# Kernel tuning notes

Hardware: AMD Instinct MI355X
Metric: run time of the kernel (lower is better)

Reference implementation:

```python
import jax, jax.numpy as jnp
import numpy as np

# NOTE: in the original SelfAttention.forward, the selected/softmaxed/dropped
# attention `attn` is NEVER used: the output is `torch.matmul(attn_cont, value)`
# with the RAW pre-mask, pre-softmax, unscaled scores. The AutoSelectAttention /
# softmax / dropout branch is dead code w.r.t. the module output, so the faithful
# forward is out = proj_out( (Q K^T) V ) per head.

B, M, HID, K = 2, 2048, 1024, 16
D = HID // K


def setup_inputs() -> dict:
    key = jax.random.key(0)
    ks = jax.random.split(key, 6)
    s = 1.0 / np.sqrt(HID)
    return {
        "h": jax.random.normal(ks[0], (B, M, HID), jnp.float32),
        "Wq": jax.random.normal(ks[1], (HID, HID), jnp.float32) * s,
        "Wk": jax.random.normal(ks[2], (HID, HID), jnp.float32) * s,
        "Wv": jax.random.normal(ks[3], (HID, HID), jnp.float32) * s,
        "Wspan": jax.random.normal(ks[4], (2 * K, HID), jnp.float32) * s,
        "Wo": jax.random.normal(ks[5], (HID, HID), jnp.float32) * s,
    }


def _heads(x, d):
    # [B, M, K*d] -> [B, K, M, d]
    b, m, _ = x.shape
    return x.reshape(b, m, K, d).transpose(0, 2, 1, 3)


def reference(h, Wq, Wk, Wv, Wspan, Wo):
    # torch Linear: y = x @ W.T  (weights stored [out, in])
    q = _heads(h @ Wq.T, D)          # [B,K,M,D]
    k = _heads(h @ Wk.T, D)          # [B,K,M,D]
    v = _heads(h @ Wv.T, D)          # [B,K,M,D]
    span = _heads(h @ Wspan.T, 2)    # [B,K,M,2] -- dead code in original, kept for parity
    del span
    # raw scores (attn_cont in the original)
    scores = jnp.einsum("bkmd,bknd->bkmn", q, k)      # [B,K,M,M]
    # original: out = attn_cont @ value (select/softmax branch unused)
    out = jnp.einsum("bkmn,bknd->bkmd", scores, v)    # [B,K,M,D]
    out = out.transpose(0, 2, 1, 3).reshape(B, M, HID)
    return out @ Wo.T
```

## Files before the change

### kernel.cpp

```cpp
#include <hip/hip_runtime.h>
#include <hip/hip_bf16.h>
#include <stdint.h>

typedef __hip_bfloat16 bf16_t;
typedef __attribute__((ext_vector_type(8))) __bf16 bf16x8;
typedef __attribute__((ext_vector_type(4))) float floatx4;

#define BM 128
#define BN 128
#define BK 64

__device__ inline void async_load16(const void* g, void* l) {
  __builtin_amdgcn_global_load_lds(
      (const __attribute__((address_space(1))) unsigned int*)g,
      (__attribute__((address_space(3))) unsigned int*)l,
      16, 0, 0);
}

__device__ inline void unpack8_bf16(float* dst, uint4 u) {
  const unsigned w[4] = {u.x, u.y, u.z, u.w};
#pragma unroll
  for (int p = 0; p < 4; ++p) {
    dst[2 * p]     = __uint_as_float(w[p] << 16);
    dst[2 * p + 1] = __uint_as_float(w[p] & 0xffff0000u);
  }
}

__device__ inline unsigned short bf16_bits(float f) {
  bf16_t b = __float2bfloat16(f);
  return *(const unsigned short*)&b;
}

__global__ void cvt_one(const float* __restrict__ src, bf16_t* __restrict__ dst) {
  const int i = (blockIdx.x * 256 + threadIdx.x) * 4;
  float4 f = *(const float4*)(src + i);
  union { unsigned short u[4]; uint2 v; } p;
  p.u[0] = bf16_bits(f.x); p.u[1] = bf16_bits(f.y);
  p.u[2] = bf16_bits(f.z); p.u[3] = bf16_bits(f.w);
  *(uint2*)(dst + i) = p.v;
}

__global__ void cvt_w4(const float* __restrict__ s0, const float* __restrict__ s1,
                       const float* __restrict__ s2, const float* __restrict__ s3,
                       bf16_t* __restrict__ d0, bf16_t* __restrict__ d1,
                       bf16_t* __restrict__ d2, bf16_t* __restrict__ d3) {
  const float* s; bf16_t* d;
  switch (blockIdx.y) {
    case 0: s = s0; d = d0; break;
    case 1: s = s1; d = d1; break;
    case 2: s = s2; d = d2; break;
    default: s = s3; d = d3; break;
  }
  const int i = (blockIdx.x * 256 + threadIdx.x) * 4;
  float4 f = *(const float4*)(s + i);
  union { unsigned short u[4]; uint2 v; } p;
  p.u[0] = bf16_bits(f.x); p.u[1] = bf16_bits(f.y);
  p.u[2] = bf16_bits(f.z); p.u[3] = bf16_bits(f.w);
  *(uint2*)(d + i) = p.v;
}

template <typename OutT>
__global__ __launch_bounds__(256, 2)
void gemm_nt(const bf16_t* __restrict__ A, int lda,
             const bf16_t* __restrict__ B0, const bf16_t* __restrict__ B1,
             const bf16_t* __restrict__ B2,
             OutT* __restrict__ C, int ldc, int Kdim)
{
  __shared__ alignas(16) __bf16 As[BM * BK];
  __shared__ alignas(16) __bf16 Bs[BN * BK];

  const int t = threadIdx.x;
  const int lane = t & 63;
  const int wave = t >> 6;
  const int wm = wave >> 1;
  const int wn = wave & 1;

  const int m0 = blockIdx.x * BM;
  const int nblk = blockIdx.y * BN;
  const int mat = nblk >> 10;
  const bf16_t* __restrict__ B = (mat == 0) ? B0 : ((mat == 1) ? B1 : B2);
  const int n0 = nblk & 1023;

  floatx4 acc[4][4];
#pragma unroll
  for (int i = 0; i < 4; ++i)
#pragma unroll
    for (int j = 0; j < 4; ++j)
      acc[i][j] = (floatx4){0.f, 0.f, 0.f, 0.f};

  const int srow = t >> 3;
  const int sgs = t & 7;

  for (int k0 = 0; k0 < Kdim; k0 += BK) {
#pragma unroll
    for (int r4 = 0; r4 < 4; ++r4) {
      const int row = r4 * 32 + srow;
      const int gsrc = sgs ^ (row & 7);
      async_load16(A + (size_t)(m0 + row) * lda + k0 + gsrc * 8,
                   &As[row * BK + sgs * 8]);
      async_load16(B + (size_t)(n0 + row) * Kdim + k0 + gsrc * 8,
                   &Bs[row * BK + sgs * 8]);
    }
    __syncthreads();
#pragma unroll
    for (int ks = 0; ks < 2; ++ks) {
      bf16x8 af[4], bfv[4];
#pragma unroll
      for (int i = 0; i < 4; ++i) {
        const int row = wm * 64 + i * 16 + (lane & 15);
        const int g = ks * 4 + (lane >> 4);
        af[i] = *(const bf16x8*)&As[row * BK + (g ^ (row & 7)) * 8];
      }
#pragma unroll
      for (int j = 0; j < 4; ++j) {
        const int row = wn * 64 + j * 16 + (lane & 15);
        const int g = ks * 4 + (lane >> 4);
        bfv[j] = *(const bf16x8*)&Bs[row * BK + (g ^ (row & 7)) * 8];
      }
#pragma unroll
      for (int i = 0; i < 4; ++i)
#pragma unroll
        for (int j = 0; j < 4; ++j)
          acc[i][j] = __builtin_amdgcn_mfma_f32_16x16x32_bf16(
              af[i], bfv[j], acc[i][j], 0, 0, 0);
    }
    __syncthreads();
  }

  const int ccol = lane & 15;
  const int crow = (lane >> 4) * 4;
#pragma unroll
  for (int i = 0; i < 4; ++i) {
#pragma unroll
    for (int j = 0; j < 4; ++j) {
      const int gcol = nblk + wn * 64 + j * 16 + ccol;
      const int growb = m0 + wm * 64 + i * 16 + crow;
#pragma unroll
      for (int r = 0; r < 4; ++r) {
        float v = acc[i][j][r];
        if constexpr (__is_same(OutT, bf16_t))
          C[(size_t)(growb + r) * ldc + gcol] = __float2bfloat16(v);
        else
          C[(size_t)(growb + r) * ldc + gcol] = v;
      }
    }
  }
}

__global__ __launch_bounds__(256)
void ktv_kernel(const bf16_t* __restrict__ qkv, float* __restrict__ S)
{
  __shared__ float Kf[32][64];
  __shared__ float Vf[32][64];
  const int bh = blockIdx.x;
  const int b = bh >> 4, hh = bh & 15;
  const int mc = blockIdx.y;
  const int t = threadIdx.x;
  const int d0 = (t & 15) * 4;
  const int e0 = (t >> 4) * 4;

  const bf16_t* kbase = qkv + (size_t)b * 2048 * 3072 + 1024 + hh * 64;
  const bf16_t* vbase = kbase + 1024;

  float acc[4][4];
#pragma unroll
  for (int i = 0; i < 4; ++i)
#pragma unroll
    for (int j = 0; j < 4; ++j) acc[i][j] = 0.f;

  const int sr = t >> 3;
  const int sc = (t & 7) * 8;

  for (int m0 = mc * 256; m0 < mc * 256 + 256; m0 += 32) {
    uint4 ku = *(const uint4*)(kbase + (size_t)(m0 + sr) * 3072 + sc);
    uint4 vu = *(const uint4*)(vbase + (size_t)(m0 + sr) * 3072 + sc);
    __syncthreads();
    unpack8_bf16(&Kf[sr][sc], ku);
    unpack8_bf16(&Vf[sr][sc], vu);
    __syncthreads();
#pragma unroll
    for (int m = 0; m < 32; ++m) {
      float kv[4], vv[4];
#pragma unroll
      for (int i = 0; i < 4; ++i) kv[i] = Kf[m][d0 + i];
#pragma unroll
      for (int j = 0; j < 4; ++j) vv[j] = Vf[m][e0 + j];
#pragma unroll
      for (int i = 0; i < 4; ++i)
#pragma unroll
        for (int j = 0; j < 4; ++j) acc[i][j] += kv[i] * vv[j];
    }
  }
  float* Sp = S + (size_t)bh * 64 * 64;
#pragma unroll
  for (int i = 0; i < 4; ++i)
#pragma unroll
    for (int j = 0; j < 4; ++j)
      atomicAdd(&Sp[(d0 + i) * 64 + e0 + j], acc[i][j]);
}

__global__ __launch_bounds__(256)
void qs_kernel(const bf16_t* __restrict__ qkv, const float* __restrict__ S,
               bf16_t* __restrict__ O)
{
  __shared__ float Ss[64][64];
  const int bh = blockIdx.x;
  const int b = bh >> 4, hh = bh & 15;
  const int mt = blockIdx.y;
  const int t = threadIdx.x;

  const float* Sp = S + (size_t)bh * 4096;
  {
    float* sf = &Ss[0][0];
#pragma unroll
    for (int i = 0; i < 16; ++i) sf[t * 16 + i] = Sp[t * 16 + i];
  }
  __syncthreads();

  const int row = t >> 1;
  const int e0 = (t & 1) * 32;
  const int m = mt * 128 + row;
  const bf16_t* qp = qkv + (size_t)(b * 2048 + m) * 3072 + hh * 64;

  float acc[32];
#pragma unroll
  for (int e = 0; e < 32; ++e) acc[e] = 0.f;

  const uint4* qv = (const uint4*)qp;
#pragma unroll
  for (int c = 0; c < 8; ++c) {
    float qf[8];
    unpack8_bf16(qf, qv[c]);
#pragma unroll
    for (int p = 0; p < 8; ++p) {
      const int d = c * 8 + p;
      const float q = qf[p];
#pragma unroll
      for (int e = 0; e < 32; ++e) acc[e] += q * Ss[d][e0 + e];
    }
  }

  bf16_t* op = O + (size_t)(b * 2048 + m) * 3072 + hh * 64 + e0;
#pragma unroll
  for (int c = 0; c < 4; ++c) {
    uint4 u;
    unsigned* pu = (unsigned*)&u;
#pragma unroll
    for (int p = 0; p < 4; ++p) {
      const int e = c * 8 + p * 2;
      unsigned lo = bf16_bits(acc[e]);
      unsigned hi = bf16_bits(acc[e + 1]);
      pu[p] = lo | (hi << 16);
    }
    ((uint4*)op)[c] = u;
  }
}

extern "C" void kernel_launch(void* const* d_in, const int* in_sizes, int n_in,
                              void* d_out, int out_size, void* d_ws, size_t ws_size,
                              hipStream_t stream)
{
  const float* h  = (const float*)d_in[0];
  const float* Wq = (const float*)d_in[1];
  const float* Wk = (const float*)d_in[2];
  const float* Wv = (const float*)d_in[3];
  const float* Wo = (const float*)d_in[5];
  float* out = (float*)d_out;

  char* ws = (char*)d_ws;
  bf16_t* hb  = (bf16_t*)(ws);
  bf16_t* Wqb = (bf16_t*)(ws + (8u << 20));
  bf16_t* Wkb = (bf16_t*)(ws + (10u << 20));
  bf16_t* Wvb = (bf16_t*)(ws + (12u << 20));
  bf16_t* Wob = (bf16_t*)(ws + (14u << 20));
  bf16_t* qkv = (bf16_t*)(ws + (16u << 20));
  float*  S   = (float*) (ws + (40u << 20));

  hipMemsetAsync(S, 0, 32 * 64 * 64 * sizeof(float), stream);

  cvt_one<<<dim3(4096), 256, 0, stream>>>(h, hb);
  cvt_w4<<<dim3(1024, 4), 256, 0, stream>>>(Wq, Wk, Wv, Wo, Wqb, Wkb, Wvb, Wob);

  gemm_nt<bf16_t><<<dim3(32, 24), 256, 0, stream>>>(hb, 1024, Wqb, Wkb, Wvb, qkv, 3072, 1024);
  ktv_kernel<<<dim3(32, 8), 256, 0, stream>>>(qkv, S);
  qs_kernel<<<dim3(32, 16), 256, 0, stream>>>(qkv, S, qkv + 1024);
  gemm_nt<float><<<dim3(32, 8), 256, 0, stream>>>(qkv + 1024, 3072, Wob, Wob, Wob, out, 1024, 1024);
}
```

Baseline: 176.6 us.

## Use MFMA for Q·S and load K/V directly in K^T V reduction

```diff
diff --git a/kernel.cpp b/kernel.cpp
--- a/kernel.cpp
+++ b/kernel.cpp
@@ -15,15 +15,6 @@
       (const __attribute__((address_space(1))) unsigned int*)g,
       (__attribute__((address_space(3))) unsigned int*)l,
       16, 0, 0);
-}
-
-__device__ inline void unpack8_bf16(float* dst, uint4 u) {
-  const unsigned w[4] = {u.x, u.y, u.z, u.w};
-#pragma unroll
-  for (int p = 0; p < 4; ++p) {
-    dst[2 * p]     = __uint_as_float(w[p] << 16);
-    dst[2 * p + 1] = __uint_as_float(w[p] & 0xffff0000u);
-  }
 }
 
 __device__ inline unsigned short bf16_bits(float f) {
@@ -147,11 +138,9 @@
   }
 }
 
-__global__ __launch_bounds__(256)
-void ktv_kernel(const bf16_t* __restrict__ qkv, float* __restrict__ S)
+__global__ __launch_bounds__(256, 2)
+void ktv_direct(const bf16_t* __restrict__ qkv, float* __restrict__ St)
 {
-  __shared__ float Kf[32][64];
-  __shared__ float Vf[32][64];
   const int bh = blockIdx.x;
   const int b = bh >> 4, hh = bh & 15;
   const int mc = blockIdx.y;
@@ -159,100 +148,123 @@
   const int d0 = (t & 15) * 4;
   const int e0 = (t >> 4) * 4;
 
-  const bf16_t* kbase = qkv + (size_t)b * 2048 * 3072 + 1024 + hh * 64;
-  const bf16_t* vbase = kbase + 1024;
+  const bf16_t* kb = qkv + (size_t)b * 2048 * 3072 + 1024 + hh * 64;
+  const bf16_t* vb = kb + 1024;
 
   float acc[4][4];
 #pragma unroll
-  for (int i = 0; i < 4; ++i)
-#pragma unroll
-    for (int j = 0; j < 4; ++j) acc[i][j] = 0.f;
-
-  const int sr = t >> 3;
-  const int sc = (t & 7) * 8;
-
-  for (int m0 = mc * 256; m0 < mc * 256 + 256; m0 += 32) {
-    uint4 ku = *(const uint4*)(kbase + (size_t)(m0 + sr) * 3072 + sc);
-    uint4 vu = *(const uint4*)(vbase + (size_t)(m0 + sr) * 3072 + sc);
-    __syncthreads();
-    unpack8_bf16(&Kf[sr][sc], ku);
-    unpack8_bf16(&Vf[sr][sc], vu);
-    __syncthreads();
-#pragma unroll
-    for (int m = 0; m < 32; ++m) {
-      float kv[4], vv[4];
-#pragma unroll
-      for (int i = 0; i < 4; ++i) kv[i] = Kf[m][d0 + i];
-#pragma unroll
-      for (int j = 0; j < 4; ++j) vv[j] = Vf[m][e0 + j];
-#pragma unroll
-      for (int i = 0; i < 4; ++i)
-#pragma unroll
-        for (int j = 0; j < 4; ++j) acc[i][j] += kv[i] * vv[j];
-    }
-  }
-  float* Sp = S + (size_t)bh * 64 * 64;
-#pragma unroll
-  for (int i = 0; i < 4; ++i)
+  for (int j = 0; j < 4; ++j)
+#pragma unroll
+    for (int i = 0; i < 4; ++i) acc[j][i] = 0.f;
+
+  const int mend = mc * 128 + 128;
+#pragma unroll 4
+  for (int m = mc * 128; m < mend; ++m) {
+    const uint2 ku = *(const uint2*)(kb + (size_t)m * 3072 + d0);
+    const uint2 vu = *(const uint2*)(vb + (size_t)m * 3072 + e0);
+    float kf[4], vf[4];
+    kf[0] = __uint_as_float(ku.x << 16); kf[1] = __uint_as_float(ku.x & 0xffff0000u);
+    kf[2] = __uint_as_float(ku.y << 16); kf[3] = __uint_as_float(ku.y & 0xffff0000u);
+    vf[0] = __uint_as_float(vu.x << 16); vf[1] = __uint_as_float(vu.x & 0xffff0000u);
+    vf[2] = __uint_as_float(vu.y << 16); vf[3] = __uint_as_float(vu.y & 0xffff0000u);
 #pragma unroll
     for (int j = 0; j < 4; ++j)
-      atomicAdd(&Sp[(d0 + i) * 64 + e0 + j], acc[i][j]);
-}
-
-__global__ __launch_bounds__(256)
-void qs_kernel(const bf16_t* __restrict__ qkv, const float* __restrict__ S,
-               bf16_t* __restrict__ O)
+#pragma unroll
+      for (int i = 0; i < 4; ++i) acc[j][i] += vf[j] * kf[i];
+  }
+  float* Sp = St + (size_t)bh * 4096;
+#pragma unroll
+  for (int j = 0; j < 4; ++j)
+#pragma unroll
+    for (int i = 0; i < 4; ++i)
+      unsafeAtomicAdd(&Sp[(e0 + j) * 64 + (d0 + i)], acc[j][i]);
+}
+
+__global__ __launch_bounds__(256, 2)
+void qs_mfma(const bf16_t* __restrict__ qkv, const float* __restrict__ St,
+             bf16_t* __restrict__ O)
 {
-  __shared__ float Ss[64][64];
+  __shared__ alignas(16) __bf16 Qs[128 * 64];
+  __shared__ alignas(16) __bf16 Sb[64 * 64];
+
+  const int t = threadIdx.x;
+  const int lane = t & 63;
+  const int wave = t >> 6;
   const int bh = blockIdx.x;
   const int b = bh >> 4, hh = bh & 15;
   const int mt = blockIdx.y;
-  const int t = threadIdx.x;
-
-  const float* Sp = S + (size_t)bh * 4096;
+
+  const bf16_t* qbase = qkv + (size_t)(b * 2048 + mt * 128) * 3072 + hh * 64;
+  const int srow = t >> 3;
+  const int sgs = t & 7;
+#pragma unroll
+  for (int r4 = 0; r4 < 4; ++r4) {
+    const int row = r4 * 32 + srow;
+    const int gsrc = sgs ^ (row & 7);
+    async_load16(qbase + (size_t)row * 3072 + gsrc * 8, &Qs[row * 64 + sgs * 8]);
+  }
   {
-    float* sf = &Ss[0][0];
-#pragma unroll
-    for (int i = 0; i < 16; ++i) sf[t * 16 + i] = Sp[t * 16 + i];
+    const int r = t >> 2;
+    const int g0 = (t & 3) * 2;
+    const float* sp = St + (size_t)bh * 4096 + r * 64;
+#pragma unroll
+    for (int gg = 0; gg < 2; ++gg) {
+      const int g = g0 + gg;
+      const int gs = g ^ (r & 7);
+      const float4 f0 = *(const float4*)(sp + gs * 8);
+      const float4 f1 = *(const float4*)(sp + gs * 8 + 4);
+      union { unsigned short u[8]; uint4 v; } pk;
+      pk.u[0] = bf16_bits(f0.x); pk.u[1] = bf16_bits(f0.y);
+      pk.u[2] = bf16_bits(f0.z); pk.u[3] = bf16_bits(f0.w);
+      pk.u[4] = bf16_bits(f1.x); pk.u[5] = bf16_bits(f1.y);
+      pk.u[6] = bf16_bits(f1.z); pk.u[7] = bf16_bits(f1.w);
+      *(uint4*)&Sb[r * 64 + g * 8] = pk.v;
+    }
   }
   __syncthreads();
 
-  const int row = t >> 1;
-  const int e0 = (t & 1) * 32;
-  const int m = mt * 128 + row;
-  const bf16_t* qp = qkv + (size_t)(b * 2048 + m) * 3072 + hh * 64;
-
-  float acc[32];
-#pragma unroll
-  for (int e = 0; e < 32; ++e) acc[e] = 0.f;
-
-  const uint4* qv = (const uint4*)qp;
-#pragma unroll
-  for (int c = 0; c < 8; ++c) {
-    float qf[8];
-    unpack8_bf16(qf, qv[c]);
-#pragma unroll
-    for (int p = 0; p < 8; ++p) {
-      const int d = c * 8 + p;
-      const float q = qf[p];
-#pragma unroll
-      for (int e = 0; e < 32; ++e) acc[e] += q * Ss[d][e0 + e];
-    }
-  }
-
-  bf16_t* op = O + (size_t)(b * 2048 + m) * 3072 + hh * 64 + e0;
-#pragma unroll
-  for (int c = 0; c < 4; ++c) {
-    uint4 u;
-    unsigned* pu = (unsigned*)&u;
-#pragma unroll
-    for (int p = 0; p < 4; ++p) {
-      const int e = c * 8 + p * 2;
-      unsigned lo = bf16_bits(acc[e]);
-      unsigned hi = bf16_bits(acc[e + 1]);
-      pu[p] = lo | (hi << 16);
-    }
-    ((uint4*)op)[c] = u;
+  floatx4 acc[2][4];
+#pragma unroll
+  for (int i = 0; i < 2; ++i)
+#pragma unroll
+    for (int j = 0; j < 4; ++j)
+      acc[i][j] = (floatx4){0.f, 0.f, 0.f, 0.f};
+
+#pragma unroll
+  for (int ks = 0; ks < 2; ++ks) {
+    bf16x8 af[2], bfv[4];
+#pragma unroll
+    for (int i = 0; i < 2; ++i) {
+      const int row = wave * 32 + i * 16 + (lane & 15);
+      const int g = ks * 4 + (lane >> 4);
+      af[i] = *(const bf16x8*)&Qs[row * 64 + (g ^ (row & 7)) * 8];
+    }
+#pragma unroll
+    for (int j = 0; j < 4; ++j) {
+      const int row = j * 16 + (lane & 15);
+      const int g = ks * 4 + (lane >> 4);
+      bfv[j] = *(const bf16x8*)&Sb[row * 64 + (g ^ (row & 7)) * 8];
+    }
+#pragma unroll
+    for (int i = 0; i < 2; ++i)
+#pragma unroll
+      for (int j = 0; j < 4; ++j)
+        acc[i][j] = __builtin_amdgcn_mfma_f32_16x16x32_bf16(
+            af[i], bfv[j], acc[i][j], 0, 0, 0);
+  }
+
+  const int ccol = lane & 15;
+  const int crow = (lane >> 4) * 4;
+#pragma unroll
+  for (int i = 0; i < 2; ++i) {
+#pragma unroll
+    for (int j = 0; j < 4; ++j) {
+      const int e = hh * 64 + j * 16 + ccol;
+      const int mrow = mt * 128 + wave * 32 + i * 16 + crow;
+#pragma unroll
+      for (int r = 0; r < 4; ++r)
+        O[(size_t)(b * 2048 + mrow + r) * 3072 + e] = __float2bfloat16(acc[i][j][r]);
+    }
   }
 }
 
@@ -274,15 +286,15 @@
   bf16_t* Wvb = (bf16_t*)(ws + (12u << 20));
   bf16_t* Wob = (bf16_t*)(ws + (14u << 20));
   bf16_t* qkv = (bf16_t*)(ws + (16u << 20));
-  float*  S   = (float*) (ws + (40u << 20));
-
-  hipMemsetAsync(S, 0, 32 * 64 * 64 * sizeof(float), stream);
+  float*  St  = (float*) (ws + (40u << 20));
+
+  hipMemsetAsync(St, 0, 32 * 64 * 64 * sizeof(float), stream);
 
   cvt_one<<<dim3(4096), 256, 0, stream>>>(h, hb);
   cvt_w4<<<dim3(1024, 4), 256, 0, stream>>>(Wq, Wk, Wv, Wo, Wqb, Wkb, Wvb, Wob);
 
   gemm_nt<bf16_t><<<dim3(32, 24), 256, 0, stream>>>(hb, 1024, Wqb, Wkb, Wvb, qkv, 3072, 1024);
-  ktv_kernel<<<dim3(32, 8), 256, 0, stream>>>(qkv, S);
-  qs_kernel<<<dim3(32, 16), 256, 0, stream>>>(qkv, S, qkv + 1024);
+  ktv_direct<<<dim3(32, 16), 256, 0, stream>>>(qkv, St);
+  qs_mfma<<<dim3(32, 16), 256, 0, stream>>>(qkv, St, qkv + 1024);
   gemm_nt<float><<<dim3(32, 8), 256, 0, stream>>>(qkv + 1024, 3072, Wob, Wob, Wob, out, 1024, 1024);
 }
```

Result: slower. 189.2 us (+7.2%).
